# Kernel optimization log

Measured on AMD Instinct MI355X. Metric: run time of the kernel, lower is better.

## Reference

```python
import jax, jax.numpy as jnp
import numpy as np

N_NODES = 50000
N_EDGES = 800000
IN_CH = 128
OUT_CH = 64
SELF_LOOP_W = 2.0  # improved=True in GCNConv


def setup_inputs() -> dict:
    key = jax.random.key(0)
    k1, k2, k3, k4 = jax.random.split(key, 4)
    x = jax.random.normal(k1, (N_NODES, IN_CH), dtype=jnp.float32)
    edge_index = jax.random.randint(k2, (2, N_EDGES), 0, N_NODES, dtype=jnp.int64)
    edge_weight = jax.random.uniform(k3, (N_EDGES,), dtype=jnp.float32)
    W = jax.random.normal(k4, (IN_CH, OUT_CH), dtype=jnp.float32) / np.sqrt(IN_CH)
    b = jnp.zeros((OUT_CH,), dtype=jnp.float32)
    return {"x": x, "edge_index": edge_index, "edge_weight": edge_weight, "W": W, "b": b}


def reference(x, edge_index, edge_weight, W, b):
    # Only the first GCNConv layer runs (the torch loop returns after k=0).
    N = x.shape[0]
    row, col = edge_index[0], edge_index[1]  # source, target

    # gcn_norm with add_self_loops=True, improved=True (fill value 2.0)
    loop_idx = jnp.arange(N, dtype=edge_index.dtype)
    row_f = jnp.concatenate([row, loop_idx])
    col_f = jnp.concatenate([col, loop_idx])
    ew_f = jnp.concatenate([edge_weight, jnp.full((N,), SELF_LOOP_W, dtype=edge_weight.dtype)])

    deg = jax.ops.segment_sum(ew_f, col_f, num_segments=N)          # [N]
    dinv = jnp.where(deg > 0, jax.lax.rsqrt(deg), 0.0)
    norm = dinv[row_f] * ew_f * dinv[col_f]                          # [E+N]

    # linear transform then normalized sparse aggregation
    xw = x @ W                                                       # [N, out]
    msg = norm[:, None] * xw[row_f]                                  # [E+N, out] gather
    out = jax.ops.segment_sum(msg, col_f, num_segments=N)           # [N, out] scatter-add
    return out + b
```

## Files before the change

kernel.cpp:

```cpp
#include <hip/hip_runtime.h>

constexpr int N    = 50000;
constexpr int E    = 800000;
constexpr int CIN  = 128;
constexpr int COUT = 64;
constexpr float SELF_LOOP_W = 2.0f;

constexpr int NB   = (N + 63) / 64;
constexpr int CAP  = 1536;
constexpr int EPB  = 2048;
constexpr int PBLK = (E + EPB - 1) / EPB;

typedef float          vfloat4  __attribute__((ext_vector_type(4)));
typedef int            vint2    __attribute__((ext_vector_type(2)));
typedef int            vint4    __attribute__((ext_vector_type(4)));
typedef unsigned short vushort4 __attribute__((ext_vector_type(4)));

__device__ __forceinline__ unsigned short f2bf(float f) {
    unsigned int u = __float_as_uint(f);
    u += 0x7FFFu + ((u >> 16) & 1u);
    return (unsigned short)(u >> 16);
}
__device__ __forceinline__ float bf2f(unsigned short h) {
    return __uint_as_float(((unsigned int)h) << 16);
}

__global__ __launch_bounds__(512) void partition_kernel(const int* __restrict__ row,
                                                        const int* __restrict__ col,
                                                        const float* __restrict__ ew,
                                                        int* __restrict__ bcur,
                                                        vint2* __restrict__ pk) {
    __shared__ int lhist[NB];
    __shared__ int lbase[NB];
    const int t  = threadIdx.x;
    const int e  = blockIdx.x * EPB + t * 4;
    const bool valid = (e < E);

    for (int i = t; i < NB; i += 512) lhist[i] = 0;
    __syncthreads();

    vint4 c4;
    if (valid) {
        c4 = *(const vint4*)(col + e);
        #pragma unroll
        for (int u = 0; u < 4; ++u) atomicAdd(&lhist[c4[u] >> 6], 1);
    }
    __syncthreads();

    for (int i = t; i < NB; i += 512) {
        int h = lhist[i];
        if (h > 0) lbase[i] = i * CAP + atomicAdd(&bcur[i], h);
    }
    __syncthreads();

    if (valid) {
        vint4   r4 = *(const vint4*)(row + e);
        vfloat4 w4 = *(const vfloat4*)(ew + e);
        #pragma unroll
        for (int u = 0; u < 4; ++u) {
            int c   = c4[u];
            int bkt = c >> 6;
            int p   = atomicAdd(&lbase[bkt], 1);
            if (p < (bkt + 1) * CAP) {
                vint2 v;
                v.x = r4[u] | ((c & 63) << 20);
                v.y = __float_as_int(w4[u]);
                pk[p] = v;
            }
        }
    }
}

__global__ __launch_bounds__(256) void xw_deg_kernel(const float* __restrict__ x,
                                                     const float* __restrict__ W,
                                                     const int* __restrict__ bcur,
                                                     const vint2* __restrict__ pk,
                                                     unsigned short* __restrict__ xwh,
                                                     float* __restrict__ dinv) {
    __shared__ __align__(16) float xs[64][132];
    __shared__ float ldeg[64];

    const int t    = threadIdx.x;
    const int b    = blockIdx.x;
    const int base = b * 64;

    #pragma unroll
    for (int i = 0; i < 8; ++i) {
        int f4  = i * 256 + t;
        int r   = f4 >> 5;
        int c4  = f4 & 31;
        int node = base + r;
        if (node >= N) node = N - 1;
        vfloat4 v = *(const vfloat4*)(x + (size_t)node * CIN + c4 * 4);
        *(vfloat4*)&xs[r][c4 * 4] = v;
    }
    if (t < 64) ldeg[t] = 0.f;
    __syncthreads();

    const int tc = t & 15;
    const int tn = t >> 4;

    float acc[4][4];
    #pragma unroll
    for (int i = 0; i < 4; ++i)
        #pragma unroll
        for (int j = 0; j < 4; ++j) acc[i][j] = 0.f;

    const float* Wp = W + tc * 4;
    #pragma unroll 4
    for (int k = 0; k < CIN; k += 4) {
        vfloat4 b0 = *(const vfloat4*)(Wp + (size_t)(k + 0) * COUT);
        vfloat4 b1 = *(const vfloat4*)(Wp + (size_t)(k + 1) * COUT);
        vfloat4 b2 = *(const vfloat4*)(Wp + (size_t)(k + 2) * COUT);
        vfloat4 b3 = *(const vfloat4*)(Wp + (size_t)(k + 3) * COUT);
        #pragma unroll
        for (int i = 0; i < 4; ++i) {
            vfloat4 a = *(const vfloat4*)&xs[tn * 4 + i][k];
            #pragma unroll
            for (int j = 0; j < 4; ++j)
                acc[i][j] += a[0] * b0[j] + a[1] * b1[j] + a[2] * b2[j] + a[3] * b3[j];
        }
    }

    #pragma unroll
    for (int i = 0; i < 4; ++i) {
        int node = base + tn * 4 + i;
        if (node >= N) continue;
        vushort4 hv;
        #pragma unroll
        for (int j = 0; j < 4; ++j) hv[j] = f2bf(acc[i][j]);
        *(vushort4*)(xwh + (size_t)node * COUT + tc * 4) = hv;
    }

    const int pbase = b * CAP;
    const int cnt   = min(bcur[b], CAP);
    for (int j = t; j < cnt; j += 256) {
        vint2 v = pk[pbase + j];
        atomicAdd(&ldeg[(v.x >> 20) & 63], __int_as_float(v.y));
    }
    __syncthreads();
    int node = base + t;
    if (t < 64 && node < N) dinv[node] = rsqrtf(SELF_LOOP_W + ldeg[t]);
}

__global__ __launch_bounds__(512) void aggregate_kernel(const int* __restrict__ bcur,
                                                        const vint2* __restrict__ pk,
                                                        const float* __restrict__ dinv,
                                                        const unsigned short* __restrict__ xwh,
                                                        const float* __restrict__ bias,
                                                        float* __restrict__ out) {
    __shared__ int   rawx[CAP];
    __shared__ float rawn[CAP];
    __shared__ int   s_r[CAP];
    __shared__ float s_n[CAP];
    __shared__ int   lhist[64], lofs[64], lcur[64];

    const int t    = threadIdx.x;
    const int lane = t & 63;
    const int wv   = t >> 6;
    const int b    = blockIdx.x;
    const int base = b * CAP;
    const int cnt  = min(bcur[b], CAP);

    if (t < 64) lhist[t] = 0;
    __syncthreads();

    for (int j = t; j < cnt; j += 512) {
        vint2 v = pk[base + j];
        rawx[j] = v.x;
        rawn[j] = __int_as_float(v.y) * dinv[v.x & 0xFFFFF];
        atomicAdd(&lhist[(v.x >> 20) & 63], 1);
    }
    __syncthreads();

    if (t < 64) {
        int v = lhist[t];
        int s = v;
        #pragma unroll
        for (int d = 1; d < 64; d <<= 1) {
            int u = __shfl_up(s, d);
            if (lane >= d) s += u;
        }
        lofs[t] = s - v;
        lcur[t] = s - v;
    }
    __syncthreads();

    for (int j = t; j < cnt; j += 512) {
        int xv = rawx[j];
        int p  = atomicAdd(&lcur[(xv >> 20) & 63], 1);
        s_r[p] = xv & 0xFFFFF;
        s_n[p] = rawn[j];
    }
    __syncthreads();

    const int q  = lane >> 4;
    const int c4 = lane & 15;

    for (int nd = wv; nd < 64; nd += 8) {
        int node = b * 64 + nd;
        if (node >= N) continue;
        int s0 = lofs[nd];
        int e0 = s0 + lhist[nd];

        float a0 = 0.f, a1 = 0.f, a2 = 0.f, a3 = 0.f;
        for (int i = s0; i < e0; i += 16) {
            int rr[4]; float nn[4]; vushort4 vv[4];
            #pragma unroll
            for (int u = 0; u < 4; ++u) {
                int j = i + 4 * u + q;
                bool ok = (j < e0);
                rr[u] = ok ? s_r[j] : s_r[s0];
                nn[u] = ok ? s_n[j] : 0.f;
            }
            #pragma unroll
            for (int u = 0; u < 4; ++u)
                vv[u] = *(const vushort4*)(xwh + (size_t)rr[u] * COUT + c4 * 4);
            #pragma unroll
            for (int u = 0; u < 4; ++u) {
                a0 += nn[u] * bf2f(vv[u][0]);
                a1 += nn[u] * bf2f(vv[u][1]);
                a2 += nn[u] * bf2f(vv[u][2]);
                a3 += nn[u] * bf2f(vv[u][3]);
            }
        }
        a0 += __shfl_xor(a0, 16); a0 += __shfl_xor(a0, 32);
        a1 += __shfl_xor(a1, 16); a1 += __shfl_xor(a1, 32);
        a2 += __shfl_xor(a2, 16); a2 += __shfl_xor(a2, 32);
        a3 += __shfl_xor(a3, 16); a3 += __shfl_xor(a3, 32);

        if (q == 0) {
            float dc = dinv[node];
            float s2 = SELF_LOOP_W * dc * dc;
            vushort4 sh = *(const vushort4*)(xwh + (size_t)node * COUT + c4 * 4);
            vfloat4  bv = *(const vfloat4*)(bias + c4 * 4);
            vfloat4  o;
            o[0] = dc * a0 + s2 * bf2f(sh[0]) + bv[0];
            o[1] = dc * a1 + s2 * bf2f(sh[1]) + bv[1];
            o[2] = dc * a2 + s2 * bf2f(sh[2]) + bv[2];
            o[3] = dc * a3 + s2 * bf2f(sh[3]) + bv[3];
            *(vfloat4*)(out + (size_t)node * COUT + c4 * 4) = o;
        }
    }
}

extern "C" void kernel_launch(void* const* d_in, const int* in_sizes, int n_in,
                              void* d_out, int out_size, void* d_ws, size_t ws_size,
                              hipStream_t stream) {
    const float* x  = (const float*)d_in[0];
    const int*   ei = (const int*)d_in[1];
    const float* ew = (const float*)d_in[2];
    const float* W  = (const float*)d_in[3];
    const float* b  = (const float*)d_in[4];
    float* out = (float*)d_out;

    unsigned short* xwh  = (unsigned short*)d_ws;
    float*          dinv = (float*)(xwh + (size_t)N * COUT);
    int*            bcur = (int*)(dinv + N);
    vint2*          pk   = (vint2*)(bcur + NB + 2);

    const int* rowp = ei;
    const int* colp = ei + E;

    hipMemsetAsync(bcur, 0, NB * sizeof(int), stream);
    partition_kernel<<<PBLK, 512, 0, stream>>>(rowp, colp, ew, bcur, pk);
    xw_deg_kernel   <<<NB, 256, 0, stream>>>(x, W, bcur, pk, xwh, dinv);
    aggregate_kernel<<<NB, 512, 0, stream>>>(bcur, pk, dinv, xwh, b, out);
}
```

Measured before the change: 151.2 us.

## Fuse edge partitioning and XW GEMM into one heterogeneous launch

Merges the partition kernel and the XW/degree kernel into a single launch where the first NB blocks compute the bf16 XW product and the remaining blocks bucket edges. Degree is now accumulated with global float atomics during partitioning, and the rsqrt is deferred into the aggregate kernel. This removes one kernel launch and the serial dependency between partitioning and the GEMM, letting both run concurrently. In exchange it adds 800k global atomics on a degree array and recomputes rsqrt per edge in aggregation.

```diff
diff --git a/kernel.cpp b/kernel.cpp
--- a/kernel.cpp
+++ b/kernel.cpp
@@ -25,127 +25,137 @@
     return __uint_as_float(((unsigned int)h) << 16);
 }
 
-__global__ __launch_bounds__(512) void partition_kernel(const int* __restrict__ row,
-                                                        const int* __restrict__ col,
-                                                        const float* __restrict__ ew,
-                                                        int* __restrict__ bcur,
-                                                        vint2* __restrict__ pk) {
-    __shared__ int lhist[NB];
-    __shared__ int lbase[NB];
-    const int t  = threadIdx.x;
-    const int e  = blockIdx.x * EPB + t * 4;
-    const bool valid = (e < E);
-
-    for (int i = t; i < NB; i += 512) lhist[i] = 0;
-    __syncthreads();
-
-    vint4 c4;
-    if (valid) {
-        c4 = *(const vint4*)(col + e);
-        #pragma unroll
-        for (int u = 0; u < 4; ++u) atomicAdd(&lhist[c4[u] >> 6], 1);
-    }
-    __syncthreads();
-
-    for (int i = t; i < NB; i += 512) {
-        int h = lhist[i];
-        if (h > 0) lbase[i] = i * CAP + atomicAdd(&bcur[i], h);
-    }
-    __syncthreads();
-
-    if (valid) {
-        vint4   r4 = *(const vint4*)(row + e);
-        vfloat4 w4 = *(const vfloat4*)(ew + e);
-        #pragma unroll
-        for (int u = 0; u < 4; ++u) {
-            int c   = c4[u];
-            int bkt = c >> 6;
-            int p   = atomicAdd(&lbase[bkt], 1);
-            if (p < (bkt + 1) * CAP) {
-                vint2 v;
-                v.x = r4[u] | ((c & 63) << 20);
-                v.y = __float_as_int(w4[u]);
-                pk[p] = v;
-            }
-        }
-    }
-}
-
-__global__ __launch_bounds__(256) void xw_deg_kernel(const float* __restrict__ x,
-                                                     const float* __restrict__ W,
-                                                     const int* __restrict__ bcur,
-                                                     const vint2* __restrict__ pk,
-                                                     unsigned short* __restrict__ xwh,
-                                                     float* __restrict__ dinv) {
-    __shared__ __align__(16) float xs[64][132];
-    __shared__ float ldeg[64];
-
-    const int t    = threadIdx.x;
-    const int b    = blockIdx.x;
-    const int base = b * 64;
-
-    #pragma unroll
-    for (int i = 0; i < 8; ++i) {
-        int f4  = i * 256 + t;
-        int r   = f4 >> 5;
-        int c4  = f4 & 31;
-        int node = base + r;
-        if (node >= N) node = N - 1;
-        vfloat4 v = *(const vfloat4*)(x + (size_t)node * CIN + c4 * 4);
-        *(vfloat4*)&xs[r][c4 * 4] = v;
-    }
-    if (t < 64) ldeg[t] = 0.f;
-    __syncthreads();
-
-    const int tc = t & 15;
-    const int tn = t >> 4;
-
-    float acc[4][4];
-    #pragma unroll
-    for (int i = 0; i < 4; ++i)
-        #pragma unroll
-        for (int j = 0; j < 4; ++j) acc[i][j] = 0.f;
-
-    const float* Wp = W + tc * 4;
-    #pragma unroll 4
-    for (int k = 0; k < CIN; k += 4) {
-        vfloat4 b0 = *(const vfloat4*)(Wp + (size_t)(k + 0) * COUT);
-        vfloat4 b1 = *(const vfloat4*)(Wp + (size_t)(k + 1) * COUT);
-        vfloat4 b2 = *(const vfloat4*)(Wp + (size_t)(k + 2) * COUT);
-        vfloat4 b3 = *(const vfloat4*)(Wp + (size_t)(k + 3) * COUT);
+__global__ __launch_bounds__(256) void fused_pxw_kernel(
+        const int* __restrict__ row, const int* __restrict__ col,
+        const float* __restrict__ ew, const float* __restrict__ x,
+        const float* __restrict__ W,
+        int* __restrict__ bcur, float* __restrict__ deg,
+        vint2* __restrict__ pk, unsigned short* __restrict__ xwh) {
+    __shared__ union __align__(16) U {
+        struct { int lhist[NB]; int lbase[NB]; } p;
+        float xs[64][132];
+    } sh;
+
+    const int t = threadIdx.x;
+
+    if ((int)blockIdx.x < NB) {
+        const int b    = blockIdx.x;
+        const int base = b * 64;
+
+        #pragma unroll
+        for (int i = 0; i < 8; ++i) {
+            int f4  = i * 256 + t;
+            int r   = f4 >> 5;
+            int c4  = f4 & 31;
+            int node = base + r;
+            if (node >= N) node = N - 1;
+            *(vfloat4*)&sh.xs[r][c4 * 4] =
+                *(const vfloat4*)(x + (size_t)node * CIN + c4 * 4);
+        }
+        __syncthreads();
+
+        const int tc = t & 15;
+        const int tn = t >> 4;
+
+        float acc[4][4];
+        #pragma unroll
+        for (int i = 0; i < 4; ++i)
+            #pragma unroll
+            for (int j = 0; j < 4; ++j) acc[i][j] = 0.f;
+
+        const float* Wp = W + tc * 4;
+        #pragma unroll 4
+        for (int k = 0; k < CIN; k += 4) {
+            vfloat4 b0 = *(const vfloat4*)(Wp + (size_t)(k + 0) * COUT);
+            vfloat4 b1 = *(const vfloat4*)(Wp + (size_t)(k + 1) * COUT);
+            vfloat4 b2 = *(const vfloat4*)(Wp + (size_t)(k + 2) * COUT);
+            vfloat4 b3 = *(const vfloat4*)(Wp + (size_t)(k + 3) * COUT);
+            #pragma unroll
+            for (int i = 0; i < 4; ++i) {
+                vfloat4 a = *(const vfloat4*)&sh.xs[tn * 4 + i][k];
+                #pragma unroll
+                for (int j = 0; j < 4; ++j)
+                    acc[i][j] += a[0] * b0[j] + a[1] * b1[j] + a[2] * b2[j] + a[3] * b3[j];
+            }
+        }
+
         #pragma unroll
         for (int i = 0; i < 4; ++i) {
-            vfloat4 a = *(const vfloat4*)&xs[tn * 4 + i][k];
-            #pragma unroll
-            for (int j = 0; j < 4; ++j)
-                acc[i][j] += a[0] * b0[j] + a[1] * b1[j] + a[2] * b2[j] + a[3] * b3[j];
-        }
-    }
-
-    #pragma unroll
-    for (int i = 0; i < 4; ++i) {
-        int node = base + tn * 4 + i;
-        if (node >= N) continue;
-        vushort4 hv;
-        #pragma unroll
-        for (int j = 0; j < 4; ++j) hv[j] = f2bf(acc[i][j]);
-        *(vushort4*)(xwh + (size_t)node * COUT + tc * 4) = hv;
-    }
-
-    const int pbase = b * CAP;
-    const int cnt   = min(bcur[b], CAP);
-    for (int j = t; j < cnt; j += 256) {
-        vint2 v = pk[pbase + j];
-        atomicAdd(&ldeg[(v.x >> 20) & 63], __int_as_float(v.y));
-    }
-    __syncthreads();
-    int node = base + t;
-    if (t < 64 && node < N) dinv[node] = rsqrtf(SELF_LOOP_W + ldeg[t]);
+            int node = base + tn * 4 + i;
+            if (node >= N) continue;
+            vushort4 hv;
+            #pragma unroll
+            for (int j = 0; j < 4; ++j) hv[j] = f2bf(acc[i][j]);
+            *(vushort4*)(xwh + (size_t)node * COUT + tc * 4) = hv;
+        }
+    } else {
+        const int pb = blockIdx.x - NB;
+        const int e  = pb * EPB + t * 8;
+        const bool valid = (e < E);
+
+        for (int i = t; i < NB; i += 256) sh.p.lhist[i] = 0;
+        __syncthreads();
+
+        vint4 ca, cb;
+        vfloat4 wa, wb;
+        if (valid) {
+            ca = *(const vint4*)(col + e);
+            cb = *(const vint4*)(col + e + 4);
+            wa = *(const vfloat4*)(ew + e);
+            wb = *(const vfloat4*)(ew + e + 4);
+            #pragma unroll
+            for (int u = 0; u < 4; ++u) {
+                atomicAdd(&sh.p.lhist[ca[u] >> 6], 1);
+                atomicAdd(&deg[ca[u]], wa[u]);
+            }
+            #pragma unroll
+            for (int u = 0; u < 4; ++u) {
+                atomicAdd(&sh.p.lhist[cb[u] >> 6], 1);
+                atomicAdd(&deg[cb[u]], wb[u]);
+            }
+        }
+        __syncthreads();
+
+        for (int i = t; i < NB; i += 256) {
+            int h = sh.p.lhist[i];
+            if (h > 0) sh.p.lbase[i] = i * CAP + atomicAdd(&bcur[i], h);
+        }
+        __syncthreads();
+
+        if (valid) {
+            vint4 ra = *(const vint4*)(row + e);
+            vint4 rb = *(const vint4*)(row + e + 4);
+            #pragma unroll
+            for (int u = 0; u < 4; ++u) {
+                int c   = ca[u];
+                int bkt = c >> 6;
+                int p   = atomicAdd(&sh.p.lbase[bkt], 1);
+                if (p < (bkt + 1) * CAP) {
+                    vint2 v;
+                    v.x = ra[u] | ((c & 63) << 20);
+                    v.y = __float_as_int(wa[u]);
+                    pk[p] = v;
+                }
+            }
+            #pragma unroll
+            for (int u = 0; u < 4; ++u) {
+                int c   = cb[u];
+                int bkt = c >> 6;
+                int p   = atomicAdd(&sh.p.lbase[bkt], 1);
+                if (p < (bkt + 1) * CAP) {
+                    vint2 v;
+                    v.x = rb[u] | ((c & 63) << 20);
+                    v.y = __float_as_int(wb[u]);
+                    pk[p] = v;
+                }
+            }
+        }
+    }
 }
 
 __global__ __launch_bounds__(512) void aggregate_kernel(const int* __restrict__ bcur,
                                                         const vint2* __restrict__ pk,
-                                                        const float* __restrict__ dinv,
+                                                        const float* __restrict__ deg,
                                                         const unsigned short* __restrict__ xwh,
                                                         const float* __restrict__ bias,
                                                         float* __restrict__ out) {
@@ -168,7 +178,8 @@
     for (int j = t; j < cnt; j += 512) {
         vint2 v = pk[base + j];
         rawx[j] = v.x;
-        rawn[j] = __int_as_float(v.y) * dinv[v.x & 0xFFFFF];
+        float dg = deg[v.x & 0xFFFFF];
+        rawn[j] = __int_as_float(v.y) * rsqrtf(SELF_LOOP_W + dg);
         atomicAdd(&lhist[(v.x >> 20) & 63], 1);
     }
     __syncthreads();
@@ -230,7 +241,7 @@
         a3 += __shfl_xor(a3, 16); a3 += __shfl_xor(a3, 32);
 
         if (q == 0) {
-            float dc = dinv[node];
+            float dc = rsqrtf(SELF_LOOP_W + deg[node]);
             float s2 = SELF_LOOP_W * dc * dc;
             vushort4 sh = *(const vushort4*)(xwh + (size_t)node * COUT + c4 * 4);
             vfloat4  bv = *(const vfloat4*)(bias + c4 * 4);
@@ -255,15 +266,15 @@
     float* out = (float*)d_out;
 
     unsigned short* xwh  = (unsigned short*)d_ws;
-    float*          dinv = (float*)(xwh + (size_t)N * COUT);
-    int*            bcur = (int*)(dinv + N);
+    float*          deg  = (float*)(xwh + (size_t)N * COUT);
+    int*            bcur = (int*)(deg + N);
     vint2*          pk   = (vint2*)(bcur + NB + 2);
 
     const int* rowp = ei;
     const int* colp = ei + E;
 
-    hipMemsetAsync(bcur, 0, NB * sizeof(int), stream);
-    partition_kernel<<<PBLK, 512, 0, stream>>>(rowp, colp, ew, bcur, pk);
-    xw_deg_kernel   <<<NB, 256, 0, stream>>>(x, W, bcur, pk, xwh, dinv);
-    aggregate_kernel<<<NB, 512, 0, stream>>>(bcur, pk, dinv, xwh, b, out);
-}
+    hipMemsetAsync(deg, 0, (size_t)(N + NB + 2) * sizeof(int), stream);
+    fused_pxw_kernel<<<NB + PBLK, 256, 0, stream>>>(rowp, colp, ew, x, W,
+                                                    bcur, deg, pk, xwh);
+    aggregate_kernel<<<NB, 512, 0, stream>>>(bcur, pk, deg, xwh, b, out);
+}
```

Result: slower. 163.0 us (+7.8%).
